# Kernel optimization log

Measured on AMD Instinct MI355X. Metric: run time of the kernel, lower is better.

Reference implementation:

```python
import jax, jax.numpy as jnp
import numpy as np

B, T = 16, 16384
K, D, H = 512, 64, 64
COMMIT = 0.25
LN_EPS = 1e-5


def setup_inputs() -> dict:
    key = jax.random.key(0)
    ks = jax.random.split(key, 4)
    t = jax.random.randint(ks[0], (B, T, 1), 0, K, dtype=jnp.int32)
    W1 = jax.random.normal(ks[1], (1, H), dtype=jnp.float32) * 0.5
    b1 = jnp.zeros((H,), dtype=jnp.float32)
    ln_g = jnp.ones((H,), dtype=jnp.float32)
    ln_b = jnp.zeros((H,), dtype=jnp.float32)
    W2 = jax.random.normal(ks[2], (H, D), dtype=jnp.float32) * (1.0 / np.sqrt(H))
    b2 = jnp.zeros((D,), dtype=jnp.float32)
    # torch init: uniform(-1/K, 1/K)
    codebook = jax.random.uniform(ks[3], (K, D), dtype=jnp.float32,
                                  minval=-1.0 / K, maxval=1.0 / K)
    return {"t": t, "W1": W1, "b1": b1, "ln_g": ln_g, "ln_b": ln_b,
            "W2": W2, "b2": b2, "codebook": codebook}


def _encoder(t, W1, b1, ln_g, ln_b, W2, b2):
    norm_t = t.astype(jnp.float32) / (K - 1) * 2.0 - 1.0  # [B,T,1]
    h = norm_t @ W1 + b1                                   # [B,T,H]
    mu = jnp.mean(h, axis=-1, keepdims=True)
    var = jnp.mean(jnp.square(h - mu), axis=-1, keepdims=True)
    h = (h - mu) * jax.lax.rsqrt(var + LN_EPS) * ln_g + ln_b
    h = jax.nn.relu(h)
    return h @ W2 + b2                                     # [B,T,D]


def reference(t, W1, b1, ln_g, ln_b, W2, b2, codebook):
    z = _encoder(t, W1, b1, ln_g, ln_b, W2, b2)            # [B,T,D]
    flat_z = z.reshape(-1, D)                               # [N,D]
    # squared distances: ||z||^2 - 2 z.e^T + ||e||^2  -> [N,K]
    dist = (jnp.sum(flat_z * flat_z, axis=1, keepdims=True)
            - 2.0 * flat_z @ codebook.T
            + jnp.sum(codebook * codebook, axis=1))
    idx = jnp.argmin(dist, axis=1)                          # [N]
    quantized = codebook[idx]                               # [N,D]
    sg = jax.lax.stop_gradient
    loss = (jnp.mean(jnp.square(quantized - sg(flat_z)))
            + COMMIT * jnp.mean(jnp.square(sg(quantized) - flat_z)))
    q = flat_z + sg(quantized - flat_z)                     # straight-through
    return q.reshape(z.shape), idx.reshape(z.shape[0], -1), loss
```

## Files before the change

kernel.cpp:

```cpp
#include <hip/hip_runtime.h>

#define Kc 512
#define Dc 64
#define Hc 64
#define Bc 16
#define Tc 16384
#define Nt (Bc * Tc)
#define LN_EPS 1e-5f
#define LOSS_SCALE (1.25f / 16777216.0f)

#define GATHER_BLOCKS 4096
#define GATHER_THREADS 256
#define GATHER_ITERS 4

__global__ __launch_bounds__(256) void precompute_kernel(
    const float* __restrict__ W1, const float* __restrict__ b1,
    const float* __restrict__ ln_g, const float* __restrict__ ln_b,
    const float* __restrict__ W2, const float* __restrict__ b2,
    const float* __restrict__ cb,
    float* __restrict__ q_table, float* __restrict__ idxf_table,
    float* __restrict__ d2_table)
{
    const int v   = blockIdx.x;
    const int tid = threadIdx.x;
    const int lane = tid & 63;
    const int wave = tid >> 6;

    __shared__ float s_h[Hc];
    __shared__ __align__(16) float s_z[Dc];
    __shared__ float s_bd[4];
    __shared__ int   s_bk[4];
    __shared__ int   s_win;
    __shared__ float s_wd;

    if (tid < 64) {
        const float norm_t = (float)v * (2.0f / (float)(Kc - 1)) - 1.0f;
        float h = norm_t * W1[lane] + b1[lane];

        float s = h;
        #pragma unroll
        for (int o = 32; o > 0; o >>= 1) s += __shfl_xor(s, o);
        const float mu = s * (1.0f / (float)Hc);
        const float d = h - mu;
        float vs = d * d;
        #pragma unroll
        for (int o = 32; o > 0; o >>= 1) vs += __shfl_xor(vs, o);
        const float var = vs * (1.0f / (float)Hc);
        float hn = d * rsqrtf(var + LN_EPS) * ln_g[lane] + ln_b[lane];
        hn = fmaxf(hn, 0.0f);
        s_h[lane] = hn;
        __builtin_amdgcn_s_waitcnt(0);
        float z = b2[lane];
        #pragma unroll
        for (int hh = 0; hh < Hc; ++hh) z = fmaf(s_h[hh], W2[hh * Dc + lane], z);
        s_z[lane] = z;
    }
    __syncthreads();

    const float4* cb4 = (const float4*)cb;
    const float4 zz = ((const float4*)s_z)[lane & 15];
    const int rowgrp = lane >> 4;

    float best_d = 3.4e38f;
    int best_k = 0;
    const int base = wave * 2048;
    #pragma unroll 4
    for (int i = 0; i < 32; ++i) {
        const float4 e = cb4[base + i * 64 + lane];
        float d0 = zz.x - e.x, d1 = zz.y - e.y, d2 = zz.z - e.z, d3 = zz.w - e.w;
        float pd = d0 * d0;
        pd = fmaf(d1, d1, pd); pd = fmaf(d2, d2, pd); pd = fmaf(d3, d3, pd);
        pd += __shfl_xor(pd, 1);
        pd += __shfl_xor(pd, 2);
        pd += __shfl_xor(pd, 4);
        pd += __shfl_xor(pd, 8);
        const int k = wave * 128 + i * 4 + rowgrp;
        if (pd < best_d) { best_d = pd; best_k = k; }
    }
    #pragma unroll
    for (int o = 32; o > 0; o >>= 1) {
        const float od = __shfl_xor(best_d, o);
        const int   ok = __shfl_xor(best_k, o);
        if (od < best_d || (od == best_d && ok < best_k)) { best_d = od; best_k = ok; }
    }
    if (lane == 0) { s_bd[wave] = best_d; s_bk[wave] = best_k; }
    __syncthreads();
    if (tid == 0) {
        float bd = s_bd[0]; int bk = s_bk[0];
        #pragma unroll
        for (int w = 1; w < 4; ++w) {
            const float od = s_bd[w]; const int ok = s_bk[w];
            if (od < bd || (od == bd && ok < bk)) { bd = od; bk = ok; }
        }
        s_win = bk; s_wd = bd;
    }
    __syncthreads();

    if (tid < 64) q_table[v * Dc + tid] = cb[s_win * Dc + tid];
    if (tid == 0) { idxf_table[v] = (float)s_win; d2_table[v] = s_wd; }
}

__global__ __launch_bounds__(GATHER_THREADS) void gather_kernel(
    const int* __restrict__ t, const float* __restrict__ q_table,
    const float* __restrict__ idxf_table, const float* __restrict__ d2_table,
    float* __restrict__ out_q, float* __restrict__ out_idx,
    float* __restrict__ partials)
{
    const int tid = threadIdx.x;
    const int g0  = blockIdx.x * GATHER_THREADS + tid;
    const int stride = GATHER_BLOCKS * GATHER_THREADS;
    const int part  = g0 & 15;

    int tvs[GATHER_ITERS];
    #pragma unroll
    for (int i = 0; i < GATHER_ITERS; ++i)
        tvs[i] = t[(g0 + i * stride) >> 4];

    float4 qs[GATHER_ITERS];
    #pragma unroll
    for (int i = 0; i < GATHER_ITERS; ++i)
        qs[i] = ((const float4*)q_table)[(tvs[i] << 4) + part];

    #pragma unroll
    for (int i = 0; i < GATHER_ITERS; ++i)
        ((float4*)out_q)[g0 + i * stride] = qs[i];

    float lsum = 0.0f;
    if (part == 0) {
        #pragma unroll
        for (int i = 0; i < GATHER_ITERS; ++i) {
            const int token = (g0 + i * stride) >> 4;
            out_idx[token] = idxf_table[tvs[i]];
            lsum += d2_table[tvs[i]];
        }
    }

    #pragma unroll
    for (int o = 32; o > 0; o >>= 1) lsum += __shfl_xor(lsum, o);
    __shared__ float s_partial[4];
    if ((tid & 63) == 0) s_partial[tid >> 6] = lsum;
    __syncthreads();
    if (tid == 0)
        partials[blockIdx.x] =
            s_partial[0] + s_partial[1] + s_partial[2] + s_partial[3];
}

__global__ __launch_bounds__(256) void loss_reduce_kernel(
    const float* __restrict__ partials, float* __restrict__ out_loss)
{
    const int tid = threadIdx.x;
    float s = 0.0f;
    #pragma unroll
    for (int i = 0; i < GATHER_BLOCKS / 256; ++i)
        s += partials[i * 256 + tid];
    #pragma unroll
    for (int o = 32; o > 0; o >>= 1) s += __shfl_xor(s, o);
    __shared__ float s_partial[4];
    if ((tid & 63) == 0) s_partial[tid >> 6] = s;
    __syncthreads();
    if (tid == 0)
        out_loss[0] = (s_partial[0] + s_partial[1] + s_partial[2] + s_partial[3])
                      * LOSS_SCALE;
}

extern "C" void kernel_launch(void* const* d_in, const int* in_sizes, int n_in,
                              void* d_out, int out_size, void* d_ws, size_t ws_size,
                              hipStream_t stream) {
    const int*   t        = (const int*)d_in[0];
    const float* W1       = (const float*)d_in[1];
    const float* b1       = (const float*)d_in[2];
    const float* ln_g     = (const float*)d_in[3];
    const float* ln_b     = (const float*)d_in[4];
    const float* W2       = (const float*)d_in[5];
    const float* b2       = (const float*)d_in[6];
    const float* codebook = (const float*)d_in[7];

    float* out      = (float*)d_out;
    float* out_q    = out;
    float* out_idx  = out + (size_t)Nt * Dc;
    float* out_loss = out_idx + Nt;

    float* ws        = (float*)d_ws;
    float* q_table   = ws;
    float* idxf_tab  = ws + Kc * Dc;
    float* d2_tab    = idxf_tab + Kc;
    float* partials  = d2_tab + Kc;

    precompute_kernel<<<Kc, 256, 0, stream>>>(
        W1, b1, ln_g, ln_b, W2, b2, codebook,
        q_table, idxf_tab, d2_tab);

    gather_kernel<<<GATHER_BLOCKS, GATHER_THREADS, 0, stream>>>(
        t, q_table, idxf_tab, d2_tab, out_q, out_idx, partials);

    loss_reduce_kernel<<<1, 256, 0, stream>>>(partials, out_loss);
}
```

Measured before the change: 104.3 us.

## Split gather into separate quantized-vector and index/loss kernels

The fused gather kernel, in which only one lane in 16 handled index writes and loss sums, is split in two. One kernel does a pure one-float4-per-thread copy of the quantized vectors, with a thread per output float4. A second small kernel handles token indices and per-wave loss partials, with each thread covering several tokens. This removes divergent index and loss work from the bandwidth-bound copy, at the cost of an extra launch and a second read of t.

Result: slower. 107.9 us (+3.4%).

```diff
diff --git a/kernel.cpp b/kernel.cpp
--- a/kernel.cpp
+++ b/kernel.cpp
@@ -9,9 +9,10 @@
 #define LN_EPS 1e-5f
 #define LOSS_SCALE (1.25f / 16777216.0f)
 
-#define GATHER_BLOCKS 4096
-#define GATHER_THREADS 256
-#define GATHER_ITERS 4
+#define QG_BLOCKS 16384
+#define IL_BLOCKS 256
+#define IL_TOKENS_PER_THREAD 4
+#define N_PARTIALS (IL_BLOCKS * 4)
 
 __global__ __launch_bounds__(256) void precompute_kernel(
     const float* __restrict__ W1, const float* __restrict__ b1,
@@ -100,49 +101,34 @@
     if (tid == 0) { idxf_table[v] = (float)s_win; d2_table[v] = s_wd; }
 }
 
-__global__ __launch_bounds__(GATHER_THREADS) void gather_kernel(
+__global__ __launch_bounds__(256) void qgather_kernel(
     const int* __restrict__ t, const float* __restrict__ q_table,
-    const float* __restrict__ idxf_table, const float* __restrict__ d2_table,
-    float* __restrict__ out_q, float* __restrict__ out_idx,
-    float* __restrict__ partials)
+    float* __restrict__ out_q)
 {
-    const int tid = threadIdx.x;
-    const int g0  = blockIdx.x * GATHER_THREADS + tid;
-    const int stride = GATHER_BLOCKS * GATHER_THREADS;
-    const int part  = g0 & 15;
+    const int g     = blockIdx.x * 256 + threadIdx.x;
+    const int tv    = t[g >> 4];
+    const int part  = g & 15;
+    ((float4*)out_q)[g] = ((const float4*)q_table)[(tv << 4) + part];
+}
 
-    int tvs[GATHER_ITERS];
+__global__ __launch_bounds__(256) void idxloss_kernel(
+    const int* __restrict__ t, const float* __restrict__ idxf_table,
+    const float* __restrict__ d2_table,
+    float* __restrict__ out_idx, float* __restrict__ partials)
+{
+    const int tid0 = blockIdx.x * 256 + threadIdx.x;
+    float lsum = 0.0f;
     #pragma unroll
-    for (int i = 0; i < GATHER_ITERS; ++i)
-        tvs[i] = t[(g0 + i * stride) >> 4];
-
-    float4 qs[GATHER_ITERS];
-    #pragma unroll
-    for (int i = 0; i < GATHER_ITERS; ++i)
-        qs[i] = ((const float4*)q_table)[(tvs[i] << 4) + part];
-
-    #pragma unroll
-    for (int i = 0; i < GATHER_ITERS; ++i)
-        ((float4*)out_q)[g0 + i * stride] = qs[i];
-
-    float lsum = 0.0f;
-    if (part == 0) {
-        #pragma unroll
-        for (int i = 0; i < GATHER_ITERS; ++i) {
-            const int token = (g0 + i * stride) >> 4;
-            out_idx[token] = idxf_table[tvs[i]];
-            lsum += d2_table[tvs[i]];
-        }
+    for (int i = 0; i < IL_TOKENS_PER_THREAD; ++i) {
+        const int token = tid0 + i * (IL_BLOCKS * 256);
+        const int tv = t[token];
+        out_idx[token] = idxf_table[tv];
+        lsum += d2_table[tv];
     }
-
     #pragma unroll
     for (int o = 32; o > 0; o >>= 1) lsum += __shfl_xor(lsum, o);
-    __shared__ float s_partial[4];
-    if ((tid & 63) == 0) s_partial[tid >> 6] = lsum;
-    __syncthreads();
-    if (tid == 0)
-        partials[blockIdx.x] =
-            s_partial[0] + s_partial[1] + s_partial[2] + s_partial[3];
+    if ((threadIdx.x & 63) == 0)
+        partials[blockIdx.x * 4 + (threadIdx.x >> 6)] = lsum;
 }
 
 __global__ __launch_bounds__(256) void loss_reduce_kernel(
@@ -151,7 +137,7 @@
     const int tid = threadIdx.x;
     float s = 0.0f;
     #pragma unroll
-    for (int i = 0; i < GATHER_BLOCKS / 256; ++i)
+    for (int i = 0; i < N_PARTIALS / 256; ++i)
         s += partials[i * 256 + tid];
     #pragma unroll
     for (int o = 32; o > 0; o >>= 1) s += __shfl_xor(s, o);
@@ -190,8 +176,10 @@
         W1, b1, ln_g, ln_b, W2, b2, codebook,
         q_table, idxf_tab, d2_tab);
 
-    gather_kernel<<<GATHER_BLOCKS, GATHER_THREADS, 0, stream>>>(
-        t, q_table, idxf_tab, d2_tab, out_q, out_idx, partials);
+    qgather_kernel<<<QG_BLOCKS, 256, 0, stream>>>(t, q_table, out_q);
+
+    idxloss_kernel<<<IL_BLOCKS, 256, 0, stream>>>(
+        t, idxf_tab, d2_tab, out_idx, partials);
 
     loss_reduce_kernel<<<1, 256, 0, stream>>>(partials, out_loss);
 }
```

## Stage quantized lookup table in LDS and gather from shared memory

Applied to the files above, without the earlier changes.

The gather kernel is restructured so each 1024-thread block first copies the whole 512x64 quantized table (128 KB) and its 1024 token ids into LDS. Each block then handles one contiguous token range and writes output rows from LDS instead of reading the table from global memory or L2 per element. Per-wave loss partials are written directly, dropping the block-level shared reduction, while keeping the same partial count. The trade-off is a 128 KB table load per block before any store can start, and only one large block per CU, which gives little latency hiding.

Result: no change. 104.7 us (+0.4%).

```diff
diff --git a/kernel.cpp b/kernel.cpp
--- a/kernel.cpp
+++ b/kernel.cpp
@@ -9,9 +9,10 @@
 #define LN_EPS 1e-5f
 #define LOSS_SCALE (1.25f / 16777216.0f)
 
-#define GATHER_BLOCKS 4096
-#define GATHER_THREADS 256
-#define GATHER_ITERS 4
+#define QG_BLOCKS 256
+#define QG_THREADS 1024
+#define QG_ITERS 16
+#define N_PARTIALS (QG_BLOCKS * 16)
 
 __global__ __launch_bounds__(256) void precompute_kernel(
     const float* __restrict__ W1, const float* __restrict__ b1,
@@ -100,49 +101,45 @@
     if (tid == 0) { idxf_table[v] = (float)s_win; d2_table[v] = s_wd; }
 }
 
-__global__ __launch_bounds__(GATHER_THREADS) void gather_kernel(
+__global__ __launch_bounds__(QG_THREADS) void qgather_kernel(
     const int* __restrict__ t, const float* __restrict__ q_table,
     const float* __restrict__ idxf_table, const float* __restrict__ d2_table,
     float* __restrict__ out_q, float* __restrict__ out_idx,
     float* __restrict__ partials)
 {
+    __shared__ __align__(16) float s_q[Kc * Dc];
+    __shared__ int s_t[QG_THREADS];
     const int tid = threadIdx.x;
-    const int g0  = blockIdx.x * GATHER_THREADS + tid;
-    const int stride = GATHER_BLOCKS * GATHER_THREADS;
-    const int part  = g0 & 15;
 
-    int tvs[GATHER_ITERS];
+    float4* s_q4 = (float4*)s_q;
+    const float4* q4 = (const float4*)q_table;
     #pragma unroll
-    for (int i = 0; i < GATHER_ITERS; ++i)
-        tvs[i] = t[(g0 + i * stride) >> 4];
+    for (int i = 0; i < (Kc * Dc / 4) / QG_THREADS; ++i)
+        s_q4[i * QG_THREADS + tid] = q4[i * QG_THREADS + tid];
+    const int tokbase = blockIdx.x * QG_THREADS;
+    s_t[tid] = t[tokbase + tid];
+    __syncthreads();
 
-    float4 qs[GATHER_ITERS];
+    const int f4base = tokbase * 16;
+    const int part = tid & 15;
+    float lsum = 0.0f;
     #pragma unroll
-    for (int i = 0; i < GATHER_ITERS; ++i)
-        qs[i] = ((const float4*)q_table)[(tvs[i] << 4) + part];
-
-    #pragma unroll
-    for (int i = 0; i < GATHER_ITERS; ++i)
-        ((float4*)out_q)[g0 + i * stride] = qs[i];
-
-    float lsum = 0.0f;
-    if (part == 0) {
-        #pragma unroll
-        for (int i = 0; i < GATHER_ITERS; ++i) {
-            const int token = (g0 + i * stride) >> 4;
-            out_idx[token] = idxf_table[tvs[i]];
-            lsum += d2_table[tvs[i]];
+    for (int i = 0; i < QG_ITERS; ++i) {
+        const int o = i * QG_THREADS + tid;
+        const int ltok = o >> 4;
+        const int tv = s_t[ltok];
+        ((float4*)out_q)[f4base + o] = s_q4[(tv << 4) + part];
+        if (part == 0) {
+            const int token = tokbase + ltok;
+            out_idx[token] = idxf_table[tv];
+            lsum += d2_table[tv];
         }
     }
 
     #pragma unroll
     for (int o = 32; o > 0; o >>= 1) lsum += __shfl_xor(lsum, o);
-    __shared__ float s_partial[4];
-    if ((tid & 63) == 0) s_partial[tid >> 6] = lsum;
-    __syncthreads();
-    if (tid == 0)
-        partials[blockIdx.x] =
-            s_partial[0] + s_partial[1] + s_partial[2] + s_partial[3];
+    if ((tid & 63) == 0)
+        partials[blockIdx.x * (QG_THREADS / 64) + (tid >> 6)] = lsum;
 }
 
 __global__ __launch_bounds__(256) void loss_reduce_kernel(
@@ -151,7 +148,7 @@
     const int tid = threadIdx.x;
     float s = 0.0f;
     #pragma unroll
-    for (int i = 0; i < GATHER_BLOCKS / 256; ++i)
+    for (int i = 0; i < N_PARTIALS / 256; ++i)
         s += partials[i * 256 + tid];
     #pragma unroll
     for (int o = 32; o > 0; o >>= 1) s += __shfl_xor(s, o);
@@ -190,7 +187,7 @@
         W1, b1, ln_g, ln_b, W2, b2, codebook,
         q_table, idxf_tab, d2_tab);
 
-    gather_kernel<<<GATHER_BLOCKS, GATHER_THREADS, 0, stream>>>(
+    qgather_kernel<<<QG_BLOCKS, QG_THREADS, 0, stream>>>(
         t, q_table, idxf_tab, d2_tab, out_q, out_idx, partials);
 
     loss_reduce_kernel<<<1, 256, 0, stream>>>(partials, out_loss);
```
